# Optimization experiments

Measured on AMD Instinct MI355X. Metric: run time of the kernel, lower is better.

Reference implementation:

```python
import jax, jax.numpy as jnp
import numpy as np


def setup_inputs() -> dict:
    key = jax.random.key(0)
    k1, k2 = jax.random.split(key)
    imgs = jax.random.normal(k1, (16, 64, 64, 64), dtype=jnp.float32)
    # matches np.random.normal(0, 0.01, (1, inCs, outCs, filtSize, filtSize, 2))
    filts = 0.01 * jax.random.normal(k2, (1, 64, 64, 3, 3, 2), dtype=jnp.float32)
    return {"imgs": imgs, "filts": filts}


def reference(imgs, filts):
    # imgs:  [B, inC, H, W] real
    # filts: [1, inC, outC, fs, fs, 2] (real/imag planes)
    B, inC, H, W = imgs.shape
    fs = filts.shape[3]
    # zero-pad image to S = H + fs - 1 (full linear-conv FFT size)
    imgs_p = jnp.pad(imgs, ((0, 0), (0, 0), (0, fs - 1), (0, fs - 1)))
    img_f = jnp.fft.fftn(imgs_p, axes=(-2, -1))  # [B, inC, S, S] complex64
    # complex filter, padded to same FFT size
    fc = (filts[0, ..., 0] + 1j * filts[0, ..., 1]).astype(jnp.complex64)  # [inC, outC, fs, fs]
    fc_p = jnp.pad(fc, ((0, 0), (0, 0), (0, H - 1), (0, W - 1)))
    filt_f = jnp.fft.fftn(fc_p, axes=(-2, -1))  # [inC, outC, S, S]
    # Karatsuba complex multiply + sum over inC == complex contraction over inC.
    # Fused as one einsum instead of materializing [B,inC,outC,S,S] intermediates.
    out_f = jnp.einsum('bihw,iohw->bohw', img_f, filt_f)  # [B, outC, S, S]
    out = jnp.fft.ifftn(out_f, axes=(-2, -1))
    # crop [1:-1, 1:-1] and take real part, as in the torch module
    return out[:, :, 1:-1, 1:-1].real.astype(imgs.dtype)
```

## Files before the change

kernel.cpp:

```cpp
#include <hip/hip_runtime.h>


typedef _Float16 f16x8 __attribute__((ext_vector_type(8)));
typedef float    f32x4 __attribute__((ext_vector_type(4)));

#define NB 16
#define NC 64
#define NH 64
#define NW 64
#define CHUNKS 528
#define SLAB_BYTES (CHUNKS * 16)
#define WF_HALFS (9 * 2 * 4 * 64 * 8)

__global__ __launch_bounds__(256) void prep_w(const float* __restrict__ filts,
                                              _Float16* __restrict__ wf) {
    const int f = blockIdx.x * 256 + threadIdx.x;
    if (f >= WF_HALFS) return;
    const int e  = f & 7;
    const int l  = (f >> 3) & 63;
    const int n  = (f >> 9) & 3;
    const int kc = (f >> 11) & 1;
    const int t  = f >> 12;
    const int i  = kc * 32 + (l >> 4) * 8 + e;
    const int o  = n * 16 + (l & 15);
    const int ky = t / 3, kx = t % 3;
    wf[f] = (_Float16)filts[(((i * 64 + o) * 3 + ky) * 3 + kx) * 2];
}

__global__ __launch_bounds__(512, 1) void conv_direct(const float* __restrict__ imgs,
                                                      const _Float16* __restrict__ wf,
                                                      float* __restrict__ out) {
    __shared__ char lds[6 * SLAB_BYTES];
    const int bid = blockIdx.x;
    const int swz = ((bid & 7) << 5) | (bid >> 3);
    const int b   = swz >> 4;
    const int y0  = (swz & 15) << 2;
    const int tid = threadIdx.x;
    const int w   = tid >> 6;
    const int l   = tid & 63;
    const int h   = l >> 4;
    const int r   = l & 15;

    if (tid < 96) {
        const int sl  = tid >> 4;
        const int rem = tid & 15;
        const int ci  = rem >> 1;
        const int xp2 = (rem & 1) ? 65 : 0;
        const int c2  = xp2 * 8 + (ci ^ (xp2 & 7));
        f16x8 z;
        #pragma unroll
        for (int k = 0; k < 8; ++k) z[k] = (_Float16)0.f;
        *reinterpret_cast<f16x8*>(lds + sl * SLAB_BYTES + c2 * 16) = z;
    }

    #pragma unroll
    for (int j = 0; j < 6; ++j) {
        const int job = w + j * 8;
        const int sl  = job >> 3;
        const int ci  = job & 7;
        const int yy  = y0 - 1 + sl;
        float fr[8];
        if ((unsigned)yy < (unsigned)NH) {
            const float* src = imgs + (((size_t)(b * NC + ci * 8)) * NH + yy) * NW + l;
            #pragma unroll
            for (int k = 0; k < 8; ++k) fr[k] = src[(size_t)k * NH * NW];
        } else {
            #pragma unroll
            for (int k = 0; k < 8; ++k) fr[k] = 0.f;
        }
        f16x8 v;
        #pragma unroll
        for (int k = 0; k < 8; ++k) v[k] = (_Float16)fr[k];
        const int xp = l + 1;
        const int chunk = xp * 8 + (ci ^ (xp & 7));
        *reinterpret_cast<f16x8*>(lds + sl * SLAB_BYTES + chunk * 16) = v;
    }
    __syncthreads();

    const int row = w >> 1;
    const int xh  = w & 1;

    f32x4 acc[2][4];
    #pragma unroll
    for (int m = 0; m < 2; ++m)
        #pragma unroll
        for (int n = 0; n < 4; ++n)
            acc[m][n] = f32x4{0.f, 0.f, 0.f, 0.f};

    #pragma unroll
    for (int ky = 0; ky < 3; ++ky) {
        const char* slab = lds + (row + 2 - ky) * SLAB_BYTES;
        #pragma unroll
        for (int kx = 0; kx < 3; ++kx) {
            const _Float16* wft = wf + (size_t)(ky * 3 + kx) * (2 * 4 * 64 * 8);
            #pragma unroll
            for (int kc = 0; kc < 2; ++kc) {
                f16x8 a[2], bb[4];
                #pragma unroll
                for (int m = 0; m < 2; ++m) {
                    const int xp = xh * 32 + m * 16 + r + 2 - kx;
                    const int chunk = xp * 8 + (((kc << 2) + h) ^ (xp & 7));
                    a[m] = *reinterpret_cast<const f16x8*>(slab + chunk * 16);
                }
                #pragma unroll
                for (int n = 0; n < 4; ++n)
                    bb[n] = *reinterpret_cast<const f16x8*>(
                        wft + ((size_t)((kc << 2) + n) * 64 + l) * 8);
                #pragma unroll
                for (int m = 0; m < 2; ++m)
                    #pragma unroll
                    for (int n = 0; n < 4; ++n)
                        acc[m][n] = __builtin_amdgcn_mfma_f32_16x16x32_f16(a[m], bb[n], acc[m][n], 0, 0, 0);
            }
        }
    }

    const int y = y0 + row;
    #pragma unroll
    for (int m = 0; m < 2; ++m) {
        const int x0 = xh * 32 + m * 16 + h * 4;
        #pragma unroll
        for (int n = 0; n < 4; ++n) {
            const int o = n * 16 + r;
            *reinterpret_cast<f32x4*>(out + (((size_t)(b * 64 + o) * 64 + y) * 64) + x0) = acc[m][n];
        }
    }
}

extern "C" void kernel_launch(void* const* d_in, const int* in_sizes, int n_in,
                              void* d_out, int out_size, void* d_ws, size_t ws_size,
                              hipStream_t stream) {
    const float* imgs  = (const float*)d_in[0];
    const float* filts = (const float*)d_in[1];
    float* out = (float*)d_out;
    _Float16* wfb = (_Float16*)d_ws;

    hipLaunchKernelGGL(prep_w, dim3((WF_HALFS + 255) / 256), dim3(256), 0, stream, filts, wfb);
    hipLaunchKernelGGL(conv_direct, dim3(256), dim3(512), 0, stream, imgs, wfb, out);
}
```

Baseline: 20.91 us.

## Fuse weight prep into conv kernel and stage fp16 weights in LDS

```diff
diff --git a/kernel.cpp b/kernel.cpp
--- a/kernel.cpp
+++ b/kernel.cpp
@@ -10,27 +10,14 @@
 #define NW 64
 #define CHUNKS 528
 #define SLAB_BYTES (CHUNKS * 16)
+#define IMG_LDS (6 * SLAB_BYTES)
 #define WF_HALFS (9 * 2 * 4 * 64 * 8)
 
-__global__ __launch_bounds__(256) void prep_w(const float* __restrict__ filts,
-                                              _Float16* __restrict__ wf) {
-    const int f = blockIdx.x * 256 + threadIdx.x;
-    if (f >= WF_HALFS) return;
-    const int e  = f & 7;
-    const int l  = (f >> 3) & 63;
-    const int n  = (f >> 9) & 3;
-    const int kc = (f >> 11) & 1;
-    const int t  = f >> 12;
-    const int i  = kc * 32 + (l >> 4) * 8 + e;
-    const int o  = n * 16 + (l & 15);
-    const int ky = t / 3, kx = t % 3;
-    wf[f] = (_Float16)filts[(((i * 64 + o) * 3 + ky) * 3 + kx) * 2];
-}
-
-__global__ __launch_bounds__(512, 1) void conv_direct(const float* __restrict__ imgs,
-                                                      const _Float16* __restrict__ wf,
-                                                      float* __restrict__ out) {
-    __shared__ char lds[6 * SLAB_BYTES];
+__global__ __launch_bounds__(512, 1) void conv_one(const float* __restrict__ imgs,
+                                                   const float* __restrict__ filts,
+                                                   float* __restrict__ out) {
+    __shared__ char lds[IMG_LDS + WF_HALFS * 2];
+    char* wfl = lds + IMG_LDS;
     const int bid = blockIdx.x;
     const int swz = ((bid & 7) << 5) | (bid >> 3);
     const int b   = swz >> 4;
@@ -75,6 +62,23 @@
         const int chunk = xp * 8 + (ci ^ (xp & 7));
         *reinterpret_cast<f16x8*>(lds + sl * SLAB_BYTES + chunk * 16) = v;
     }
+
+    #pragma unroll
+    for (int q = 0; q < 9; ++q) {
+        const int c  = tid * 9 + q;
+        const int fl = c & 63;
+        const int n  = (c >> 6) & 3;
+        const int kc = (c >> 8) & 1;
+        const int t  = c >> 9;
+        const int o  = n * 16 + (fl & 15);
+        const int i0 = kc * 32 + (fl >> 4) * 8;
+        const float* src = filts + ((size_t)i0 * 64 + o) * 18 + t * 2;
+        f16x8 v;
+        #pragma unroll
+        for (int e = 0; e < 8; ++e)
+            v[e] = (_Float16)src[(size_t)e * 64 * 18];
+        *reinterpret_cast<f16x8*>(wfl + c * 16) = v;
+    }
     __syncthreads();
 
     const int row = w >> 1;
@@ -92,7 +96,8 @@
         const char* slab = lds + (row + 2 - ky) * SLAB_BYTES;
         #pragma unroll
         for (int kx = 0; kx < 3; ++kx) {
-            const _Float16* wft = wf + (size_t)(ky * 3 + kx) * (2 * 4 * 64 * 8);
+            const int t = ky * 3 + kx;
+            const char* wt = wfl + (size_t)t * 8192;
             #pragma unroll
             for (int kc = 0; kc < 2; ++kc) {
                 f16x8 a[2], bb[4];
@@ -105,7 +110,7 @@
                 #pragma unroll
                 for (int n = 0; n < 4; ++n)
                     bb[n] = *reinterpret_cast<const f16x8*>(
-                        wft + ((size_t)((kc << 2) + n) * 64 + l) * 8);
+                        wt + (size_t)(kc * 4 + n) * 1024 + l * 16);
                 #pragma unroll
                 for (int m = 0; m < 2; ++m)
                     #pragma unroll
@@ -133,8 +138,7 @@
     const float* imgs  = (const float*)d_in[0];
     const float* filts = (const float*)d_in[1];
     float* out = (float*)d_out;
-    _Float16* wfb = (_Float16*)d_ws;
+    (void)d_ws; (void)ws_size;
 
-    hipLaunchKernelGGL(prep_w, dim3((WF_HALFS + 255) / 256), dim3(256), 0, stream, filts, wfb);
-    hipLaunchKernelGGL(conv_direct, dim3(256), dim3(512), 0, stream, imgs, wfb, out);
+    hipLaunchKernelGGL(conv_one, dim3(256), dim3(512), 0, stream, imgs, filts, out);
 }
```

Result: slower. 47.89 us (+129.0%).
